# Kernel optimization log

Measured on AMD Instinct MI355X. Metric: run time of the kernel, lower is better.

The kernel has to match this reference:

```python
import jax, jax.numpy as jnp
import numpy as np

B, S, D, H = 4, 1024, 1024, 16
DK = D // H


def _linear_params(key, scale):
    kw, kb = jax.random.split(key)
    W = jax.random.normal(kw, (D, D), dtype=jnp.float32) * scale
    b = jax.random.normal(kb, (D,), dtype=jnp.float32) * 0.01
    return W, b


def setup_inputs() -> dict:
    key = jax.random.key(0)
    ks = jax.random.split(key, 12)
    scale = 1.0 / np.sqrt(D)
    inp = {
        "query": jax.random.normal(ks[0], (B, S, D), dtype=jnp.float32),
        "key": jax.random.normal(ks[1], (B, S, D), dtype=jnp.float32),
        "value": jax.random.normal(ks[2], (B, S, D), dtype=jnp.float32),
        "time_k": jax.random.normal(ks[3], (B, S, D), dtype=jnp.float32),
        "time_v": jax.random.normal(ks[4], (B, S, D), dtype=jnp.float32),
        "mask": jnp.zeros((B, 1, S, S), dtype=jnp.float32),
    }
    names = ["Wq", "bq", "Wk", "bk", "Wv", "bv", "Wtk", "btk", "Wtv", "btv", "Wm", "bm"]
    for i in range(6):
        W, b = _linear_params(ks[5 + i], scale)
        inp[names[2 * i]] = W
        inp[names[2 * i + 1]] = b
    return inp


def _split_heads(x):
    # [B,S,D] -> [B,H,S,DK]
    b, s, _ = x.shape
    return x.reshape(b, s, H, DK).transpose(0, 2, 1, 3)


def reference(query, key, value, time_k, time_v, mask,
              Wq, bq, Wk, bk, Wv, bv, Wtk, btk, Wtv, btv, Wm, bm):
    q = _split_heads(query @ Wq + bq)
    k = _split_heads(key @ Wk + bk)
    v = _split_heads(value @ Wv + bv)
    t_k = _split_heads(time_k @ Wtk + btk)
    t_v = _split_heads(time_v @ Wtv + btv)

    # scores[b,h,i,j] = q_i . k_j + t_k_i . q_j  (note second term uses q on the key axis)
    scores = jnp.einsum("bhid,bhjd->bhij", q, k) + jnp.einsum("bhid,bhjd->bhij", t_k, q)
    # module divides by sqrt(d_model) (query.size(-1)), not sqrt(d_k)
    scores = scores / jnp.sqrt(jnp.float32(D)) + mask
    probs = jax.nn.softmax(scores, axis=-1)

    # dropout is identity (p=0 / eval); squeeze(-2) is a no-op for S>1
    context = jnp.einsum("bhij,bhjd->bhid", probs, v) + jnp.einsum("bhij,bhjd->bhid", probs, t_v)
    x = context.transpose(0, 2, 1, 3).reshape(query.shape[0], -1, D)
    return x @ Wm + bm
```

## Files before the change

### kernel.cpp

```cpp
#include <hip/hip_runtime.h>
#include <hip/hip_bf16.h>
#include <cstdint>
#include <cstddef>

typedef __bf16 bf16;
typedef bf16 bf16x8 __attribute__((ext_vector_type(8)));
typedef bf16 bf16x4 __attribute__((ext_vector_type(4)));
typedef float f32x4 __attribute__((ext_vector_type(4)));
typedef unsigned int u32;

#define DEV static __device__ __forceinline__

DEV f32x4 mfma16(bf16x8 a, bf16x8 b, f32x4 c) {
    return __builtin_amdgcn_mfma_f32_16x16x32_bf16(a, b, c, 0, 0, 0);
}

DEV f32x4 shflx4(f32x4 v, int m) {
    f32x4 r;
    for (int i = 0; i < 4; ++i) r[i] = __shfl_xor(v[i], m, 64);
    return r;
}

DEV bf16x8 cvt8(const float* p) {
    float4 f0 = *(const float4*)p;
    float4 f1 = *(const float4*)(p + 4);
    bf16x8 v;
    v[0] = (bf16)f0.x; v[1] = (bf16)f0.y; v[2] = (bf16)f0.z; v[3] = (bf16)f0.w;
    v[4] = (bf16)f1.x; v[5] = (bf16)f1.y; v[6] = (bf16)f1.z; v[7] = (bf16)f1.w;
    return v;
}

DEV void glo(const bf16* g, bf16* l) {
    __builtin_amdgcn_global_load_lds(
        (const __attribute__((address_space(1))) u32*)g,
        (__attribute__((address_space(3))) u32*)l,
        16, 0, 0);
}

struct PrepArgs {
    const float* w[6];
    const float* act[5];
    bf16* wdst[6];  int wstride[6];
    bf16* adst[5];  int astride[5];
};

__global__ __launch_bounds__(256) void prep_kernel(PrepArgs p)
{
    const int z = blockIdx.z;
    const int t = threadIdx.x;
    if (z < 6) {
        __shared__ bf16 tile[64][72];
        const float* src = p.w[z];
        bf16* out = p.wdst[z];
        const int os = p.wstride[z];
        const int r = t >> 3, c8 = (t & 7) * 8;
        const int row0 = blockIdx.y * 64, col0 = blockIdx.x * 64;
        *(bf16x8*)&tile[r][c8]      = cvt8(&src[(size_t)(row0 + r) * 1024 + col0 + c8]);
        *(bf16x8*)&tile[r + 32][c8] = cvt8(&src[(size_t)(row0 + r + 32) * 1024 + col0 + c8]);
        __syncthreads();
        for (int half = 0; half < 2; ++half) {
            int rr = r + half * 32;
            bf16x8 v;
            for (int j = 0; j < 8; ++j) v[j] = tile[c8 + j][rr];
            *(bf16x8*)&out[(size_t)(col0 + rr) * os + row0 + c8] = v;
        }
    } else {
        const float* src = p.act[z - 6];
        bf16* dst = p.adst[z - 6];
        const int as = p.astride[z - 6];
        const size_t chunk = (size_t)(blockIdx.y * 16 + blockIdx.x) * 16384;
        for (int c = 0; c < 8; ++c) {
            const size_t off = chunk + (size_t)c * 2048 + (size_t)t * 8;
            const size_t row = off >> 10, col = off & 1023;
            *(bf16x8*)&dst[row * (size_t)as + col] = cvt8(&src[off]);
        }
    }
}

__global__ __launch_bounds__(256) void maskprep_kernel(
    const float* __restrict__ mask, bf16* __restrict__ maskR)
{
    const int jt = blockIdx.x, it = blockIdx.y, b = blockIdx.z;
    __shared__ bf16 Mt[128 * 72];
    const int t = threadIdx.x, lane = t & 63, w = t >> 6;
    const int ln = lane & 15, qd = lane >> 4;
    {
        const int il = t >> 1, jh = (t & 1) * 32;
        const float* src = &mask[((size_t)b * 1024 + it * 128 + il) * 1024 + jt * 64 + jh];
        *(bf16x8*)&Mt[il * 72 + jh]      = cvt8(src);
        *(bf16x8*)&Mt[il * 72 + jh + 8]  = cvt8(src + 8);
        *(bf16x8*)&Mt[il * 72 + jh + 16] = cvt8(src + 16);
        *(bf16x8*)&Mt[il * 72 + jh + 24] = cvt8(src + 24);
    }
    __syncthreads();
    bf16 m[32];
    for (int si = 0; si < 2; ++si)
        for (int jc = 0; jc < 4; ++jc)
            for (int r = 0; r < 4; ++r) {
                const int il = w * 32 + si * 16 + qd * 4 + r;
                const int jl = jc * 16 + ln;
                m[(si * 4 + jc) * 4 + r] = Mt[il * 72 + jl];
            }
    bf16* dst = &maskR[((((size_t)b * 8 + it) * 16 + jt) * 256 + t) * 32];
    for (int c = 0; c < 4; ++c)
        *(bf16x8*)&dst[c * 8] = *(const bf16x8*)&m[c * 8];
}

struct ProjArgs {
    const bf16* A[4];
    const bf16* W[4];
    const float* bias[4];
    const float* bias2[4];
    bf16* out[4];
    int vst[4];
    int nk[4];
};

__global__ __launch_bounds__(256) void proj_gemm(ProjArgs pa)
{
    const int z = blockIdx.z;
    const bf16* A = pa.A[z];
    const bf16* W = pa.W[z];
    const int nk = pa.nk[z];
    const int lda = nk << 6;
    const int m0 = blockIdx.x * 128, n0 = blockIdx.y * 128;
    __shared__ bf16 As[128 * 64];
    __shared__ bf16 Bs[128 * 64];
    const int t = threadIdx.x, lane = t & 63, w = t >> 6;
    const int ln = lane & 15, qd = lane >> 4;
    const int wm0 = (w >> 1) * 64, wn0 = (w & 1) * 64;
    const int sub0 = w * 4;
    const int rr = lane >> 3;
    const int cbs = (((lane & 7) ^ rr)) * 8;
    const int lx = ln & 7;
    f32x4 acc[4][4];
    for (int i = 0; i < 4; ++i)
        for (int j = 0; j < 4; ++j)
            acc[i][j] = (f32x4){0.f, 0.f, 0.f, 0.f};
    for (int ks = 0; ks < nk; ++ks) {
        const int bk = ks * 64;
        __syncthreads();
        for (int i = 0; i < 4; ++i) {
            const int row = (sub0 + i) * 8 + rr;
            glo(&W[(size_t)(n0 + row) * lda + bk + cbs], &Bs[(sub0 + i) * 512]);
            glo(&A[(size_t)(m0 + row) * lda + bk + cbs], &As[(sub0 + i) * 512]);
        }
        __syncthreads();
        for (int kc = 0; kc < 2; ++kc) {
            const int sg = ((kc * 4 + qd) ^ lx) * 8;
            bf16x8 af[4], bfr[4];
            for (int mi = 0; mi < 4; ++mi)
                af[mi] = *(const bf16x8*)&As[(wm0 + mi * 16 + ln) * 64 + sg];
            for (int ni = 0; ni < 4; ++ni)
                bfr[ni] = *(const bf16x8*)&Bs[(wn0 + ni * 16 + ln) * 64 + sg];
            for (int mi = 0; mi < 4; ++mi)
                for (int ni = 0; ni < 4; ++ni)
                    acc[mi][ni] = mfma16(af[mi], bfr[ni], acc[mi][ni]);
        }
    }
    const float* bias = pa.bias[z];
    const float* bias2 = pa.bias2[z];
    bf16* out = pa.out[z];
    const int vst = pa.vst[z];
    for (int ni = 0; ni < 4; ++ni) {
        const int n = n0 + wn0 + ni * 16 + ln;
        const float bv = bias[n] + (bias2 ? bias2[n] : 0.0f);
        for (int mi = 0; mi < 4; ++mi) {
            const int mbase = m0 + wm0 + mi * 16 + qd * 4;
            f32x4 v = acc[mi][ni];
            if (vst) {
                const int b = mbase >> 10, s = mbase & 1023;
                bf16x4 pk;
                for (int r = 0; r < 4; ++r) pk[r] = (bf16)(v[r] + bv);
                *(bf16x4*)&out[((size_t)(b * 1024 + n)) * 1024 + s] = pk;
            } else {
                for (int r = 0; r < 4; ++r)
                    out[(size_t)(mbase + r) * 1024 + n] = (bf16)(v[r] + bv);
            }
        }
    }
}

__global__ __launch_bounds__(256) void attn6_kernel(
    const bf16* __restrict__ Qb, const bf16* __restrict__ Kb, const bf16* __restrict__ TKb,
    const bf16* __restrict__ Vsum,
    const bf16* __restrict__ maskR, bf16* __restrict__ ctx)
{
    const int h = blockIdx.x, it = blockIdx.y, b = blockIdx.z;
    const int i0 = it * 128;
    __shared__ bf16 Ks[64 * 64];
    __shared__ bf16 QJs[64 * 64];
    __shared__ bf16 Vs[64 * 64];
    __shared__ bf16 Ps[128][68];
    const int t = threadIdx.x, lane = t & 63, w = t >> 6;
    const int ln = lane & 15, qd = lane >> 4;
    const int lx = ln & 7;
    const size_t baseQ = ((size_t)b * 1024) * 1024 + (size_t)h * 64;
    const size_t baseV = ((size_t)b * 1024 + h * 64) * 1024;

    bf16x8 qf[2][2], tkf[2][2];
    for (int si = 0; si < 2; ++si) {
        const size_t row = (size_t)(i0 + w * 32 + si * 16 + ln);
        for (int kc = 0; kc < 2; ++kc) {
            qf[si][kc]  = *(const bf16x8*)&Qb [baseQ + row * 1024 + kc * 32 + qd * 8];
            tkf[si][kc] = *(const bf16x8*)&TKb[baseQ + row * 1024 + kc * 32 + qd * 8];
        }
    }

    f32x4 O[2][4];
    f32x4 psum[2];
    for (int si = 0; si < 2; ++si) {
        psum[si] = (f32x4){0.f, 0.f, 0.f, 0.f};
        for (int dc = 0; dc < 4; ++dc) O[si][dc] = (f32x4){0.f, 0.f, 0.f, 0.f};
    }

    const float c1 = 0.045084439f;
    const float c2 = 1.442695041f;

    const size_t mtile0 = (((size_t)b * 8 + it) * 16) * 256 + t;

    for (int jt = 0; jt < 16; ++jt) {
        const int j0 = jt * 64;
        __syncthreads();
        {
            const int rr = lane >> 3;
            const int cbs = ((lane & 7) ^ rr) * 8;
            for (int i = 0; i < 6; ++i) {
                const int u = w * 6 + i;
                if (u < 8) {
                    glo(&Kb[baseQ + (size_t)(j0 + u * 8 + rr) * 1024 + cbs], &Ks[u * 512]);
                } else if (u < 16) {
                    const int s = u - 8;
                    glo(&Qb[baseQ + (size_t)(j0 + s * 8 + rr) * 1024 + cbs], &QJs[s * 512]);
                } else {
                    const int s = u - 16;
                    glo(&Vsum[baseV + (size_t)(s * 8 + rr) * 1024 + j0 + cbs], &Vs[s * 512]);
                }
            }
        }
        bf16x8 mm[4];
        {
            const bf16* mb = &maskR[(mtile0 + (size_t)jt * 256) * 32];
            for (int c = 0; c < 4; ++c) mm[c] = *(const bf16x8*)&mb[c * 8];
        }
        __syncthreads();

        f32x4 sc[2][4];
        for (int jc = 0; jc < 4; ++jc) {
            bf16x8 kf[2], qjf[2];
            for (int kc = 0; kc < 2; ++kc) {
                const int sg = ((kc * 4 + qd) ^ lx) * 8;
                kf[kc]  = *(const bf16x8*)&Ks [(jc * 16 + ln) * 64 + sg];
                qjf[kc] = *(const bf16x8*)&QJs[(jc * 16 + ln) * 64 + sg];
            }
            for (int si = 0; si < 2; ++si) {
                f32x4 a = (f32x4){0.f, 0.f, 0.f, 0.f};
                a = mfma16(qf[si][0], kf[0], a);
                a = mfma16(qf[si][1], kf[1], a);
                a = mfma16(tkf[si][0], qjf[0], a);
                a = mfma16(tkf[si][1], qjf[1], a);
                sc[si][jc] = a;
            }
        }
        for (int si = 0; si < 2; ++si) {
            const int ibl = w * 32 + si * 16 + qd * 4;
            for (int jc = 0; jc < 4; ++jc) {
                const int jl = jc * 16 + ln;
                const int e = si * 4 + jc;
                for (int r = 0; r < 4; ++r) {
                    const float mval = (float)mm[e >> 1][(e & 1) * 4 + r];
                    const float p = exp2f(fmaf(sc[si][jc][r], c1, mval * c2));
                    psum[si][r] += p;
                    Ps[ibl + r][jl] = (bf16)p;
                }
            }
        }
        for (int kc = 0; kc < 2; ++kc) {
            bf16x8 pa[2], vb[4];
            for (int si = 0; si < 2; ++si) {
                bf16x4 lo = *(const bf16x4*)&Ps[w * 32 + si * 16 + ln][kc * 32 + qd * 8];
                bf16x4 hi = *(const bf16x4*)&Ps[w * 32 + si * 16 + ln][kc * 32 + qd * 8 + 4];
                for (int e = 0; e < 4; ++e) { pa[si][e] = lo[e]; pa[si][4 + e] = hi[e]; }
            }
            for (int dc = 0; dc < 4; ++dc) {
                const int vrow = dc * 16 + ln;
                const int sg = ((kc * 4 + qd) ^ lx) * 8;
                vb[dc] = *(const bf16x8*)&Vs[vrow * 64 + sg];
            }
            for (int si = 0; si < 2; ++si)
                for (int dc = 0; dc < 4; ++dc)
                    O[si][dc] = mfma16(pa[si], vb[dc], O[si][dc]);
        }
    }

    for (int si = 0; si < 2; ++si) {
        for (int m = 1; m <= 8; m <<= 1) psum[si] += shflx4(psum[si], m);
        f32x4 rl;
        for (int r = 0; r < 4; ++r) rl[r] = 1.0f / psum[si][r];
        const int ibase = i0 + w * 32 + si * 16 + qd * 4;
        for (int dc = 0; dc < 4; ++dc) {
            const int d = h * 64 + dc * 16 + ln;
            f32x4 v = O[si][dc] * rl;
            for (int r = 0; r < 4; ++r)
                ctx[((size_t)b * 1024 + ibase + r) * 1024 + d] = (bf16)v[r];
        }
    }
}

__global__ __launch_bounds__(256) void out_gemm(
    const bf16* __restrict__ A, const bf16* __restrict__ W,
    const float* __restrict__ bias, float* __restrict__ out)
{
    const int m0 = blockIdx.x * 64, n0 = blockIdx.y * 128;
    __shared__ bf16 As[64 * 64];
    __shared__ bf16 Bs[128 * 64];
    const int t = threadIdx.x, lane = t & 63, w = t >> 6;
    const int ln = lane & 15, qd = lane >> 4;
    const int wn0 = w * 32;
    const int rr = lane >> 3;
    const int cbs = ((lane & 7) ^ rr) * 8;
    const int lx = ln & 7;
    f32x4 acc[4][2];
    for (int i = 0; i < 4; ++i)
        for (int j = 0; j < 2; ++j)
            acc[i][j] = (f32x4){0.f, 0.f, 0.f, 0.f};
    for (int ks = 0; ks < 16; ++ks) {
        const int bk = ks * 64;
        __syncthreads();
        for (int i = 0; i < 6; ++i) {
            const int u = w * 6 + i;
            if (u < 8) {
                glo(&A[(size_t)(m0 + u * 8 + rr) * 1024 + bk + cbs], &As[u * 512]);
            } else {
                const int sub = u - 8;
                glo(&W[(size_t)(n0 + sub * 8 + rr) * 1024 + bk + cbs], &Bs[sub * 512]);
            }
        }
        __syncthreads();
        for (int kc = 0; kc < 2; ++kc) {
            const int sg = ((kc * 4 + qd) ^ lx) * 8;
            bf16x8 af[4], bfr[2];
            for (int mi = 0; mi < 4; ++mi)
                af[mi] = *(const bf16x8*)&As[(mi * 16 + ln) * 64 + sg];
            for (int ni = 0; ni < 2; ++ni)
                bfr[ni] = *(const bf16x8*)&Bs[(wn0 + ni * 16 + ln) * 64 + sg];
            for (int mi = 0; mi < 4; ++mi)
                for (int ni = 0; ni < 2; ++ni)
                    acc[mi][ni] = mfma16(af[mi], bfr[ni], acc[mi][ni]);
        }
    }
    for (int ni = 0; ni < 2; ++ni) {
        const int n = n0 + wn0 + ni * 16 + ln;
        const float bv = bias[n];
        for (int mi = 0; mi < 4; ++mi) {
            const int mbase = m0 + mi * 16 + qd * 4;
            f32x4 v = acc[mi][ni];
            for (int r = 0; r < 4; ++r)
                out[(size_t)(mbase + r) * 1024 + n] = v[r] + bv;
        }
    }
}

extern "C" void kernel_launch(void* const* d_in, const int* in_sizes, int n_in,
                              void* d_out, int out_size, void* d_ws, size_t ws_size,
                              hipStream_t stream)
{
    (void)in_sizes; (void)n_in; (void)out_size; (void)ws_size;
    const float* query  = (const float*)d_in[0];
    const float* key    = (const float*)d_in[1];
    const float* value  = (const float*)d_in[2];
    const float* time_k = (const float*)d_in[3];
    const float* time_v = (const float*)d_in[4];
    const float* mask   = (const float*)d_in[5];
    const float* Wq  = (const float*)d_in[6];  const float* bq  = (const float*)d_in[7];
    const float* Wk  = (const float*)d_in[8];  const float* bk  = (const float*)d_in[9];
    const float* Wv  = (const float*)d_in[10]; const float* bv  = (const float*)d_in[11];
    const float* Wtk = (const float*)d_in[12]; const float* btk = (const float*)d_in[13];
    const float* Wtv = (const float*)d_in[14]; const float* btv = (const float*)d_in[15];
    const float* Wm  = (const float*)d_in[16]; const float* bm  = (const float*)d_in[17];

    bf16* ws = (bf16*)d_ws;
    const size_t MM = (size_t)1024 * 1024;
    bf16* WTq  = ws + 0 * MM;
    bf16* WTk  = ws + 1 * MM;
    bf16* WTtk = ws + 2 * MM;
    bf16* WTm  = ws + 3 * MM;
    bf16* WT5  = ws + 4 * MM;
    bf16* qbf  = ws + 6 * MM;
    bf16* kbf  = ws + 10 * MM;
    bf16* tkbf = ws + 14 * MM;
    bf16* A5   = ws + 18 * MM;
    bf16* Qb   = ws + 26 * MM;
    bf16* Kb   = ws + 30 * MM;
    bf16* TKb  = ws + 34 * MM;
    bf16* VsT  = ws + 38 * MM;
    bf16* ctx  = ws + 6 * MM;
    bf16* maskR = (bf16*)d_out;

    PrepArgs pp;
    pp.w[0] = Wq;  pp.wdst[0] = WTq;        pp.wstride[0] = 1024;
    pp.w[1] = Wk;  pp.wdst[1] = WTk;        pp.wstride[1] = 1024;
    pp.w[2] = Wv;  pp.wdst[2] = WT5;        pp.wstride[2] = 2048;
    pp.w[3] = Wtk; pp.wdst[3] = WTtk;       pp.wstride[3] = 1024;
    pp.w[4] = Wtv; pp.wdst[4] = WT5 + 1024; pp.wstride[4] = 2048;
    pp.w[5] = Wm;  pp.wdst[5] = WTm;        pp.wstride[5] = 1024;
    pp.act[0] = query;  pp.adst[0] = qbf;       pp.astride[0] = 1024;
    pp.act[1] = key;    pp.adst[1] = kbf;       pp.astride[1] = 1024;
    pp.act[2] = value;  pp.adst[2] = A5;        pp.astride[2] = 2048;
    pp.act[3] = time_k; pp.adst[3] = tkbf;      pp.astride[3] = 1024;
    pp.act[4] = time_v; pp.adst[4] = A5 + 1024; pp.astride[4] = 2048;
    prep_kernel<<<dim3(16, 16, 11), 256, 0, stream>>>(pp);
    maskprep_kernel<<<dim3(16, 8, 4), 256, 0, stream>>>(mask, maskR);

    ProjArgs pa;
    pa.A[0] = qbf;  pa.W[0] = WTq;  pa.bias[0] = bq;  pa.bias2[0] = nullptr;
    pa.out[0] = Qb;  pa.vst[0] = 0; pa.nk[0] = 16;
    pa.A[1] = kbf;  pa.W[1] = WTk;  pa.bias[1] = bk;  pa.bias2[1] = nullptr;
    pa.out[1] = Kb;  pa.vst[1] = 0; pa.nk[1] = 16;
    pa.A[2] = tkbf; pa.W[2] = WTtk; pa.bias[2] = btk; pa.bias2[2] = nullptr;
    pa.out[2] = TKb; pa.vst[2] = 0; pa.nk[2] = 16;
    pa.A[3] = A5;   pa.W[3] = WT5;  pa.bias[3] = bv;  pa.bias2[3] = btv;
    pa.out[3] = VsT; pa.vst[3] = 1; pa.nk[3] = 32;
    proj_gemm<<<dim3(32, 8, 4), 256, 0, stream>>>(pa);

    attn6_kernel<<<dim3(16, 8, 4), 256, 0, stream>>>(
        Qb, Kb, TKb, VsT, maskR, ctx);
    out_gemm<<<dim3(64, 8), 256, 0, stream>>>(ctx, WTm, bm, (float*)d_out);
}
```

Baseline: 316.8 us.

## Double-buffer LDS tiles in attention and output GEMM, fold mask prep into prep kernel

Adds ping-pong LDS buffers to the attention and output GEMM kernels, issuing the next tile's global-to-LDS loads before computing on the current tile, with manual vmcnt waits and barriers. This is meant to hide global load latency behind the MFMA work. Separately, the mask conversion kernel is merged into the prep kernel as extra z-slices, saving one launch. LDS use doubles, which may lower occupancy, and the hand-written waitcnt values must match the number of outstanding loads.

```diff
diff --git a/kernel.cpp b/kernel.cpp
--- a/kernel.cpp
+++ b/kernel.cpp
@@ -37,11 +37,16 @@
         16, 0, 0);
 }
 
+#define WAITB(n) asm volatile("s_waitcnt vmcnt(" #n ")\n\ts_barrier" ::: "memory")
+#define BAR()    asm volatile("s_barrier" ::: "memory")
+
 struct PrepArgs {
     const float* w[6];
     const float* act[5];
+    const float* mask;
     bf16* wdst[6];  int wstride[6];
     bf16* adst[5];  int astride[5];
+    bf16* maskR;
 };
 
 __global__ __launch_bounds__(256) void prep_kernel(PrepArgs p)
@@ -64,7 +69,7 @@
             for (int j = 0; j < 8; ++j) v[j] = tile[c8 + j][rr];
             *(bf16x8*)&out[(size_t)(col0 + rr) * os + row0 + c8] = v;
         }
-    } else {
+    } else if (z < 11) {
         const float* src = p.act[z - 6];
         bf16* dst = p.adst[z - 6];
         const int as = p.astride[z - 6];
@@ -74,36 +79,33 @@
             const size_t row = off >> 10, col = off & 1023;
             *(bf16x8*)&dst[row * (size_t)as + col] = cvt8(&src[off]);
         }
-    }
-}
-
-__global__ __launch_bounds__(256) void maskprep_kernel(
-    const float* __restrict__ mask, bf16* __restrict__ maskR)
-{
-    const int jt = blockIdx.x, it = blockIdx.y, b = blockIdx.z;
-    __shared__ bf16 Mt[128 * 72];
-    const int t = threadIdx.x, lane = t & 63, w = t >> 6;
-    const int ln = lane & 15, qd = lane >> 4;
-    {
-        const int il = t >> 1, jh = (t & 1) * 32;
-        const float* src = &mask[((size_t)b * 1024 + it * 128 + il) * 1024 + jt * 64 + jh];
-        *(bf16x8*)&Mt[il * 72 + jh]      = cvt8(src);
-        *(bf16x8*)&Mt[il * 72 + jh + 8]  = cvt8(src + 8);
-        *(bf16x8*)&Mt[il * 72 + jh + 16] = cvt8(src + 16);
-        *(bf16x8*)&Mt[il * 72 + jh + 24] = cvt8(src + 24);
-    }
-    __syncthreads();
-    bf16 m[32];
-    for (int si = 0; si < 2; ++si)
-        for (int jc = 0; jc < 4; ++jc)
-            for (int r = 0; r < 4; ++r) {
-                const int il = w * 32 + si * 16 + qd * 4 + r;
-                const int jl = jc * 16 + ln;
-                m[(si * 4 + jc) * 4 + r] = Mt[il * 72 + jl];
-            }
-    bf16* dst = &maskR[((((size_t)b * 8 + it) * 16 + jt) * 256 + t) * 32];
-    for (int c = 0; c < 4; ++c)
-        *(bf16x8*)&dst[c * 8] = *(const bf16x8*)&m[c * 8];
+    } else {
+        if (blockIdx.y >= 8) return;
+        const int jt = blockIdx.x, it = blockIdx.y, b = z - 11;
+        __shared__ bf16 Mt[128 * 72];
+        const int lane = t & 63, w = t >> 6;
+        const int ln = lane & 15, qd = lane >> 4;
+        {
+            const int il = t >> 1, jh = (t & 1) * 32;
+            const float* src = &p.mask[((size_t)b * 1024 + it * 128 + il) * 1024 + jt * 64 + jh];
+            *(bf16x8*)&Mt[il * 72 + jh]      = cvt8(src);
+            *(bf16x8*)&Mt[il * 72 + jh + 8]  = cvt8(src + 8);
+            *(bf16x8*)&Mt[il * 72 + jh + 16] = cvt8(src + 16);
+            *(bf16x8*)&Mt[il * 72 + jh + 24] = cvt8(src + 24);
+        }
+        __syncthreads();
+        bf16 m[32];
+        for (int si = 0; si < 2; ++si)
+            for (int jc = 0; jc < 4; ++jc)
+                for (int r = 0; r < 4; ++r) {
+                    const int il = w * 32 + si * 16 + qd * 4 + r;
+                    const int jl = jc * 16 + ln;
+                    m[(si * 4 + jc) * 4 + r] = Mt[il * 72 + jl];
+                }
+        bf16* dst = &p.maskR[((((size_t)b * 8 + it) * 16 + jt) * 256 + t) * 32];
+        for (int c = 0; c < 4; ++c)
+            *(bf16x8*)&dst[c * 8] = *(const bf16x8*)&m[c * 8];
+    }
 }
 
 struct ProjArgs {
@@ -188,13 +190,15 @@
 {
     const int h = blockIdx.x, it = blockIdx.y, b = blockIdx.z;
     const int i0 = it * 128;
-    __shared__ bf16 Ks[64 * 64];
-    __shared__ bf16 QJs[64 * 64];
-    __shared__ bf16 Vs[64 * 64];
+    __shared__ bf16 Ks[2][64 * 64];
+    __shared__ bf16 QJs[2][64 * 64];
+    __shared__ bf16 Vs[2][64 * 64];
     __shared__ bf16 Ps[128][68];
     const int t = threadIdx.x, lane = t & 63, w = t >> 6;
     const int ln = lane & 15, qd = lane >> 4;
     const int lx = ln & 7;
+    const int rr = lane >> 3;
+    const int cbs = ((lane & 7) ^ rr) * 8;
     const size_t baseQ = ((size_t)b * 1024) * 1024 + (size_t)h * 64;
     const size_t baseV = ((size_t)b * 1024 + h * 64) * 1024;
 
@@ -219,39 +223,47 @@
 
     const size_t mtile0 = (((size_t)b * 8 + it) * 16) * 256 + t;
 
+    auto stage = [&](int jt) {
+        const int buf = jt & 1;
+        const int j0 = jt * 64;
+        for (int i = 0; i < 6; ++i) {
+            const int u = w * 6 + i;
+            if (u < 8) {
+                glo(&Kb[baseQ + (size_t)(j0 + u * 8 + rr) * 1024 + cbs], &Ks[buf][u * 512]);
+            } else if (u < 16) {
+                const int s = u - 8;
+                glo(&Qb[baseQ + (size_t)(j0 + s * 8 + rr) * 1024 + cbs], &QJs[buf][s * 512]);
+            } else {
+                const int s = u - 16;
+                glo(&Vsum[baseV + (size_t)(s * 8 + rr) * 1024 + j0 + cbs], &Vs[buf][s * 512]);
+            }
+        }
+    };
+
+    stage(0);
+
     for (int jt = 0; jt < 16; ++jt) {
-        const int j0 = jt * 64;
-        __syncthreads();
-        {
-            const int rr = lane >> 3;
-            const int cbs = ((lane & 7) ^ rr) * 8;
-            for (int i = 0; i < 6; ++i) {
-                const int u = w * 6 + i;
-                if (u < 8) {
-                    glo(&Kb[baseQ + (size_t)(j0 + u * 8 + rr) * 1024 + cbs], &Ks[u * 512]);
-                } else if (u < 16) {
-                    const int s = u - 8;
-                    glo(&Qb[baseQ + (size_t)(j0 + s * 8 + rr) * 1024 + cbs], &QJs[s * 512]);
-                } else {
-                    const int s = u - 16;
-                    glo(&Vsum[baseV + (size_t)(s * 8 + rr) * 1024 + j0 + cbs], &Vs[s * 512]);
-                }
-            }
-        }
+        const int cur = jt & 1;
         bf16x8 mm[4];
         {
             const bf16* mb = &maskR[(mtile0 + (size_t)jt * 256) * 32];
             for (int c = 0; c < 4; ++c) mm[c] = *(const bf16x8*)&mb[c * 8];
         }
-        __syncthreads();
+        BAR();
+        if (jt < 15) {
+            stage(jt + 1);
+            WAITB(6);
+        } else {
+            WAITB(0);
+        }
 
         f32x4 sc[2][4];
         for (int jc = 0; jc < 4; ++jc) {
             bf16x8 kf[2], qjf[2];
             for (int kc = 0; kc < 2; ++kc) {
                 const int sg = ((kc * 4 + qd) ^ lx) * 8;
-                kf[kc]  = *(const bf16x8*)&Ks [(jc * 16 + ln) * 64 + sg];
-                qjf[kc] = *(const bf16x8*)&QJs[(jc * 16 + ln) * 64 + sg];
+                kf[kc]  = *(const bf16x8*)&Ks [cur][(jc * 16 + ln) * 64 + sg];
+                qjf[kc] = *(const bf16x8*)&QJs[cur][(jc * 16 + ln) * 64 + sg];
             }
             for (int si = 0; si < 2; ++si) {
                 f32x4 a = (f32x4){0.f, 0.f, 0.f, 0.f};
@@ -285,7 +297,7 @@
             for (int dc = 0; dc < 4; ++dc) {
                 const int vrow = dc * 16 + ln;
                 const int sg = ((kc * 4 + qd) ^ lx) * 8;
-                vb[dc] = *(const bf16x8*)&Vs[vrow * 64 + sg];
+                vb[dc] = *(const bf16x8*)&Vs[cur][vrow * 64 + sg];
             }
             for (int si = 0; si < 2; ++si)
                 for (int dc = 0; dc < 4; ++dc)
@@ -312,8 +324,8 @@
     const float* __restrict__ bias, float* __restrict__ out)
 {
     const int m0 = blockIdx.x * 64, n0 = blockIdx.y * 128;
-    __shared__ bf16 As[64 * 64];
-    __shared__ bf16 Bs[128 * 64];
+    __shared__ bf16 As[2][64 * 64];
+    __shared__ bf16 Bs[2][128 * 64];
     const int t = threadIdx.x, lane = t & 63, w = t >> 6;
     const int ln = lane & 15, qd = lane >> 4;
     const int wn0 = w * 32;
@@ -324,26 +336,39 @@
     for (int i = 0; i < 4; ++i)
         for (int j = 0; j < 2; ++j)
             acc[i][j] = (f32x4){0.f, 0.f, 0.f, 0.f};
-    for (int ks = 0; ks < 16; ++ks) {
+
+    auto stage = [&](int ks) {
+        const int buf = ks & 1;
         const int bk = ks * 64;
-        __syncthreads();
         for (int i = 0; i < 6; ++i) {
             const int u = w * 6 + i;
             if (u < 8) {
-                glo(&A[(size_t)(m0 + u * 8 + rr) * 1024 + bk + cbs], &As[u * 512]);
+                glo(&A[(size_t)(m0 + u * 8 + rr) * 1024 + bk + cbs], &As[buf][u * 512]);
             } else {
                 const int sub = u - 8;
-                glo(&W[(size_t)(n0 + sub * 8 + rr) * 1024 + bk + cbs], &Bs[sub * 512]);
-            }
-        }
-        __syncthreads();
+                glo(&W[(size_t)(n0 + sub * 8 + rr) * 1024 + bk + cbs], &Bs[buf][sub * 512]);
+            }
+        }
+    };
+
+    stage(0);
+
+    for (int ks = 0; ks < 16; ++ks) {
+        const int cur = ks & 1;
+        BAR();
+        if (ks < 15) {
+            stage(ks + 1);
+            WAITB(6);
+        } else {
+            WAITB(0);
+        }
         for (int kc = 0; kc < 2; ++kc) {
             const int sg = ((kc * 4 + qd) ^ lx) * 8;
             bf16x8 af[4], bfr[2];
             for (int mi = 0; mi < 4; ++mi)
-                af[mi] = *(const bf16x8*)&As[(mi * 16 + ln) * 64 + sg];
+                af[mi] = *(const bf16x8*)&As[cur][(mi * 16 + ln) * 64 + sg];
             for (int ni = 0; ni < 2; ++ni)
-                bfr[ni] = *(const bf16x8*)&Bs[(wn0 + ni * 16 + ln) * 64 + sg];
+                bfr[ni] = *(const bf16x8*)&Bs[cur][(wn0 + ni * 16 + ln) * 64 + sg];
             for (int mi = 0; mi < 4; ++mi)
                 for (int ni = 0; ni < 2; ++ni)
                     acc[mi][ni] = mfma16(af[mi], bfr[ni], acc[mi][ni]);
@@ -409,8 +434,8 @@
     pp.act[2] = value;  pp.adst[2] = A5;        pp.astride[2] = 2048;
     pp.act[3] = time_k; pp.adst[3] = tkbf;      pp.astride[3] = 1024;
     pp.act[4] = time_v; pp.adst[4] = A5 + 1024; pp.astride[4] = 2048;
-    prep_kernel<<<dim3(16, 16, 11), 256, 0, stream>>>(pp);
-    maskprep_kernel<<<dim3(16, 8, 4), 256, 0, stream>>>(mask, maskR);
+    pp.mask = mask; pp.maskR = maskR;
+    prep_kernel<<<dim3(16, 16, 15), 256, 0, stream>>>(pp);
 
     ProjArgs pa;
     pa.A[0] = qbf;  pa.W[0] = WTq;  pa.bias[0] = bq;  pa.bias2[0] = nullptr;
```

Result: no change. 315.5 us (-0.4%).
